# Kernel tuning notes

Hardware: AMD Instinct MI355X
Metric: run time of the kernel (lower is better)

The kernel has to match this reference:

```python
import jax, jax.numpy as jnp
import numpy as np

B, S, D, H, DK, F = 8, 1024, 1024, 16, 64, 4096
EPS = 1e-5


def _layer_norm(x, g, b):
    mu = jnp.mean(x, axis=-1, keepdims=True)
    var = jnp.var(x, axis=-1, keepdims=True)
    return (x - mu) * jax.lax.rsqrt(var + EPS) * g + b


def setup_inputs() -> dict:
    key = jax.random.key(0)
    ks = jax.random.split(key, 16)
    s = lambda fan: 1.0 / np.sqrt(fan)
    return {
        "src": jax.random.normal(ks[0], (B, S, D), dtype=jnp.float32),
        "Wq": jax.random.uniform(ks[1], (H, D, DK), jnp.float32, -s(D), s(D)),
        "bq": jnp.zeros((H, DK), jnp.float32),
        "Wk": jax.random.uniform(ks[2], (H, D, DK), jnp.float32, -s(D), s(D)),
        "bk": jnp.zeros((H, DK), jnp.float32),
        "Wv": jax.random.uniform(ks[3], (H, D, DK), jnp.float32, -s(D), s(D)),
        "bv": jnp.zeros((H, DK), jnp.float32),
        "Wo": jax.random.uniform(ks[4], (H * DK, D), jnp.float32, -s(H * DK), s(H * DK)),
        "bo": jnp.zeros((D,), jnp.float32),
        "g1": jnp.ones((D,), jnp.float32),
        "be1": jnp.zeros((D,), jnp.float32),
        "W1": jax.random.uniform(ks[5], (D, F), jnp.float32, -s(D), s(D)),
        "b1": jnp.zeros((F,), jnp.float32),
        "W2": jax.random.uniform(ks[6], (F, D), jnp.float32, -s(F), s(F)),
        "b2": jnp.zeros((D,), jnp.float32),
        "g2": jnp.ones((D,), jnp.float32),
        "be2": jnp.zeros((D,), jnp.float32),
    }


def reference(src, Wq, bq, Wk, bk, Wv, bv, Wo, bo, g1, be1, W1, b1, W2, b2, g2, be2):
    # Per-head projections (vectorized over the Python head loop of the original)
    q = jnp.einsum("bsd,hdk->bhsk", src, Wq) + bq[:, None, :]
    k = jnp.einsum("bsd,hdk->bhsk", src, Wk) + bk[:, None, :]
    v = jnp.einsum("bsd,hdk->bhsk", src, Wv) + bv[:, None, :]
    scale = 1.0 / jnp.sqrt(jnp.asarray(DK, src.dtype))
    scores = jnp.einsum("bhsk,bhtk->bhst", q, k) * scale  # [B,H,S,S]
    attn = jax.nn.softmax(scores, axis=-1)
    o = jnp.einsum("bhst,bhtk->bhsk", attn, v)
    # torch.cat over heads on last dim -> [B,S,H*DK] with head-major feature order
    o = o.transpose(0, 2, 1, 3).reshape(B, S, H * DK)
    attn_out = o @ Wo + bo
    x = _layer_norm(src + attn_out, g1, be1)  # dropout inactive at inference
    ff = jax.nn.relu(x @ W1 + b1) @ W2 + b2
    return _layer_norm(x + ff, g2, be2)
```

## Files before the change

kernel.cpp:

```cpp
#include <hip/hip_runtime.h>

#define Bq 8
#define Sq 1024
#define Dq 1024
#define Hq 16
#define DKq 64
#define Fq 4096
#define TOK (Bq*Sq)

typedef unsigned short u16;
typedef unsigned int u32;
typedef __bf16 bf16x8 __attribute__((ext_vector_type(8)));
typedef float  f32x4  __attribute__((ext_vector_type(4)));

__device__ __forceinline__ float bf2f(u16 u) {
  u32 x = ((u32)u) << 16;
  float f; __builtin_memcpy(&f, &x, 4); return f;
}
__device__ __forceinline__ u16 f2bf(float f) {
  u32 u; __builtin_memcpy(&u, &f, 4);
  u += 0x7fffu + ((u >> 16) & 1u);
  return (u16)(u >> 16);
}
__device__ __forceinline__ void async16(const u16* g, u16* l) {
  __builtin_amdgcn_global_load_lds(
      (__attribute__((address_space(1))) void*)(g),
      (__attribute__((address_space(3))) void*)(l), 16, 0, 0);
}
__device__ __forceinline__ u16 load_in(const void* p, long idx, u32 fp32) {
  return fp32 ? f2bf(((const float*)p)[idx]) : ((const u16*)p)[idx];
}
__device__ __forceinline__ int swzb(int row, int colb) {
  return row * 128 + (colb ^ ((row & 7) << 4));
}

struct InTab { const void* p[17]; int n[17]; };

__global__ void detect_all(InTab tab, u32* flags) {
  __shared__ int sh[3][256];
  int bi = blockIdx.x;
  const u16* buf = (const u16*)tab.p[bi];
  long n = tab.n[bi];
  long m = n < 65536 ? n : 65536;
  int t = threadIdx.x;
  int nanpat = 0, evz = 0, oddnz = 0;
  for (long i = t; i < m; i += 256) {
    u16 v = buf[i];
    if ((v & 0x7F80u) == 0x7F80u) nanpat++;
    if ((i & 1) == 0) { if (v == 0) evz++; }
    else { if (v != 0) oddnz++; }
  }
  sh[0][t] = nanpat; sh[1][t] = evz; sh[2][t] = oddnz;
  __syncthreads();
  for (int s = 128; s > 0; s >>= 1) {
    if (t < s) { sh[0][t] += sh[0][t+s]; sh[1][t] += sh[1][t+s]; sh[2][t] += sh[2][t+s]; }
    __syncthreads();
  }
  if (t == 0) {
    long half = m / 2;
    bool fp32 = (sh[0][0] > 8) ||
                (sh[1][0] > (half * 9) / 10 && sh[2][0] > (half * 9) / 10);
    flags[bi] = fp32 ? 1u : 0u;
  }
}

__global__ void diag_ws_too_small(u16* out, float code) { out[0] = f2bf(code); }

__global__ void diag_mixed(const u32* flags, void* out) {
  u32 a = flags[0];
  if (flags[1] != a || flags[7] != a || flags[11] != a || flags[13] != a) {
    if (a) ((float*)out)[0] = 3000.0f;
    else ((u16*)out)[0] = f2bf(3000.0f);
  }
}

__global__ __launch_bounds__(256) void pack_all(const void* __restrict__ Wq,
                                                const void* __restrict__ Wk,
                                                const void* __restrict__ Wv,
                                                const void* __restrict__ Wo,
                                                const void* __restrict__ W1,
                                                const void* __restrict__ W2,
                                                u16* __restrict__ Wqkv_t,
                                                u16* __restrict__ Wo_t,
                                                u16* __restrict__ W1_t,
                                                u16* __restrict__ W2_t,
                                                const u32* __restrict__ flags) {
  int id = blockIdx.x;
  const void* in; u16* out; u32 f; int R, C; long zin; int r0, c0;
  if (id < 768) {
    int w = id >> 8, t = id & 255;
    int z = t >> 4, xt = t & 15;
    in = (w == 0) ? Wq : ((w == 1) ? Wk : Wv);
    f = flags[(w == 0) ? 1 : ((w == 1) ? 3 : 5)];
    R = 1024; C = 64;
    zin = (long)z * 65536;
    out = Wqkv_t + (long)w * 1048576 + (long)z * 65536;
    r0 = xt * 64; c0 = 0;
  } else if (id < 1024) {
    int t = id - 768; int xt = t & 15, yt = t >> 4;
    in = Wo; f = flags[7]; R = 1024; C = 1024; zin = 0; out = Wo_t;
    r0 = xt * 64; c0 = yt * 64;
  } else if (id < 2048) {
    int t = id - 1024; int xt = t & 15, yt = t >> 4;
    in = W1; f = flags[11]; R = 1024; C = 4096; zin = 0; out = W1_t;
    r0 = xt * 64; c0 = yt * 64;
  } else {
    int t = id - 2048; int xt = t & 63, yt = t >> 6;
    in = W2; f = flags[13]; R = 4096; C = 1024; zin = 0; out = W2_t;
    r0 = xt * 64; c0 = yt * 64;
  }
  __shared__ u16 tile[64][65];
  int tx = threadIdx.x & 63, ty = threadIdx.x >> 6;
#pragma unroll
  for (int it = 0; it < 16; it++) {
    int row = it * 4 + ty;
    tile[row][tx] = load_in(in, zin + (long)(r0 + row) * C + (c0 + tx), f);
  }
  __syncthreads();
#pragma unroll
  for (int it = 0; it < 16; it++) {
    int cc = it * 4 + ty;
    out[(long)(c0 + cc) * R + r0 + tx] = tile[tx][cc];
  }
}

struct CvtTab { const void* p[10]; int flagidx[10]; int dstoff[10]; int n[10]; };
__global__ void cvt_small(CvtTab tab, u16* __restrict__ dst, const u32* __restrict__ flags) {
  int e = blockIdx.x;
  u32 f = flags[tab.flagidx[e]];
  const void* p = tab.p[e];
  int n = tab.n[e], o = tab.dstoff[e];
  for (int i = threadIdx.x; i < n; i += 256) dst[o + i] = load_in(p, i, f);
}

__global__ __launch_bounds__(256) void cvt_src(const void* __restrict__ in,
                                               u16* __restrict__ out,
                                               const u32* __restrict__ flag) {
  u32 f = *flag;
  long i8 = ((long)blockIdx.x * 256 + threadIdx.x) * 8;
  if (f) {
    const float4* f4 = (const float4*)((const float*)in + i8);
    float4 a = f4[0], b = f4[1];
    u16 v[8] = {f2bf(a.x), f2bf(a.y), f2bf(a.z), f2bf(a.w),
                f2bf(b.x), f2bf(b.y), f2bf(b.z), f2bf(b.w)};
    *(uint4*)(out + i8) = *(const uint4*)v;
  } else {
    *(uint4*)(out + i8) = *(const uint4*)((const u16*)in + i8);
  }
}

__global__ __launch_bounds__(256) void gemm_bt(const u16* __restrict__ A,
                                               const u16* __restrict__ Bt,
                                               const u16* __restrict__ bias,
                                               u16* __restrict__ C,
                                               int M, int N, int K, int act,
                                               int ldc) {
  __shared__ alignas(16) u16 sA[2][128 * 32];
  __shared__ alignas(16) u16 sB[2][128 * 32];
  const int tid = threadIdx.x;
  const int wv = tid >> 6, lane = tid & 63;
  const int m16 = lane & 15, quad = lane >> 4;
  const long bm = (long)blockIdx.x * 128;
  const long bn = (long)blockIdx.y * 128;
  const int wm = (wv >> 1) * 64, wn = (wv & 1) * 64;

  f32x4 acc[4][4];
#pragma unroll
  for (int i = 0; i < 4; i++)
#pragma unroll
    for (int j = 0; j < 4; j++) acc[i][j] = (f32x4){0.f, 0.f, 0.f, 0.f};

  const int row_s = tid >> 2;
  const int col_s = (tid & 3) * 8;
  const u16* gA0 = A + (bm + row_s) * (long)K + col_s;
  const u16* gA1 = gA0 + 64 * (long)K;
  const u16* gB0 = Bt + (bn + row_s) * (long)K + col_s;
  const u16* gB1 = gB0 + 64 * (long)K;

  auto stage = [&](int p, int k) {
    async16(gA0 + k, &sA[p][wv * 512]);
    async16(gA1 + k, &sA[p][2048 + wv * 512]);
    async16(gB0 + k, &sB[p][wv * 512]);
    async16(gB1 + k, &sB[p][2048 + wv * 512]);
  };
  auto compute = [&](int p) {
    bf16x8 af[4], bf_[4];
#pragma unroll
    for (int mi = 0; mi < 4; mi++)
      af[mi] = *(const bf16x8*)&sA[p][(wm + mi * 16 + m16) * 32 + quad * 8];
#pragma unroll
    for (int ni = 0; ni < 4; ni++)
      bf_[ni] = *(const bf16x8*)&sB[p][(wn + ni * 16 + m16) * 32 + quad * 8];
#pragma unroll
    for (int mi = 0; mi < 4; mi++)
#pragma unroll
      for (int ni = 0; ni < 4; ni++)
        acc[mi][ni] = __builtin_amdgcn_mfma_f32_16x16x32_bf16(af[mi], bf_[ni], acc[mi][ni], 0, 0, 0);
  };

  stage(0, 0);
  for (int k0 = 0; k0 < K; k0 += 64) {
    __syncthreads();
    if (k0 + 32 < K) stage(1, k0 + 32);
    compute(0);
    __syncthreads();
    if (k0 + 64 < K) stage(0, k0 + 64);
    compute(1);
  }

  float bv4[4];
#pragma unroll
  for (int ni = 0; ni < 4; ni++) bv4[ni] = bf2f(bias[bn + wn + ni * 16 + m16]);

#pragma unroll
  for (int mi = 0; mi < 4; mi++) {
#pragma unroll
    for (int ni = 0; ni < 4; ni++) {
      long col = bn + wn + ni * 16 + m16;
      long rowb = bm + wm + mi * 16 + quad * 4;
#pragma unroll
      for (int r = 0; r < 4; r++) {
        float v = acc[mi][ni][r] + bv4[ni];
        if (act) v = fmaxf(v, 0.f);
        C[(rowb + r) * (long)ldc + col] = f2bf(v);
      }
    }
  }
}

#define MF16 __builtin_amdgcn_mfma_f32_16x16x32_bf16

#define TILE256(BUF, NBUF, DOA, DOB, KA, KB, VMS)                              \
  {                                                                            \
                   \
    _Pragma("unroll") for (int mi = 0; mi < 4; mi++)                           \
      _Pragma("unroll") for (int kk = 0; kk < 2; kk++)                         \
        afr[mi][kk] = *(const bf16x8*)&sA[BUF][offA + mi * 1024 + kof[kk]];    \
    _Pragma("unroll") for (int ni = 0; ni < 2; ni++)                           \
      _Pragma("unroll") for (int kk = 0; kk < 2; kk++)                         \
        bfr[ni][kk] = *(const bf16x8*)&sB[BUF][offB + ni * 1024 + kof[kk]];    \
    if (DOA) stA(NBUF, 0, KA);                                                 \
    __builtin_amdgcn_s_barrier();                                              \
    asm volatile("s_waitcnt lgkmcnt(0)");                                      \
    __builtin_amdgcn_s_setprio(1);                                             \
    _Pragma("unroll") for (int kk = 0; kk < 2; kk++)                           \
      _Pragma("unroll") for (int mi = 0; mi < 4; mi++)                         \
        _Pragma("unroll") for (int ni = 0; ni < 2; ni++)                       \
          acc[mi][ni] = MF16(afr[mi][kk], bfr[ni][kk], acc[mi][ni], 0, 0, 0);  \
    __builtin_amdgcn_s_setprio(0);                                             \
    __builtin_amdgcn_s_barrier();                                              \
                                 \
    _Pragma("unroll") for (int ni = 0; ni < 2; ni++)                           \
      _Pragma("unroll") for (int kk = 0; kk < 2; kk++)                         \
        bfr[2 + ni][kk] = *(const bf16x8*)&sB[BUF][offB + (2 + ni) * 1024 + kof[kk]]; \
    if (DOA) stA(NBUF, 1, KA);                                                 \
    __builtin_amdgcn_s_barrier();                                              \
    asm volatile("s_waitcnt lgkmcnt(0)");                                      \
    __builtin_amdgcn_s_setprio(1);                                             \
    _Pragma("unroll") for (int kk = 0; kk < 2; kk++)                           \
      _Pragma("unroll") for (int mi = 0; mi < 4; mi++)                         \
        _Pragma("unroll") for (int ni = 0; ni < 2; ni++)                       \
          acc[mi][2 + ni] = MF16(afr[mi][kk], bfr[2 + ni][kk], acc[mi][2 + ni], 0, 0, 0); \
    __builtin_amdgcn_s_setprio(0);                                             \
    __builtin_amdgcn_s_barrier();                                              \
     \
    _Pragma("unroll") for (int mi = 0; mi < 4; mi++)                           \
      _Pragma("unroll") for (int kk = 0; kk < 2; kk++)                         \
        afr[mi][kk] = *(const bf16x8*)&sA[BUF][offA + (4 + mi) * 1024 + kof[kk]]; \
    if (DOB) stB(BUF, 0, KB);                                                  \
    __builtin_amdgcn_s_barrier();                                              \
    asm volatile("s_waitcnt lgkmcnt(0)");                                      \
    __builtin_amdgcn_s_setprio(1);                                             \
    _Pragma("unroll") for (int kk = 0; kk < 2; kk++)                           \
      _Pragma("unroll") for (int mi = 0; mi < 4; mi++)                         \
        _Pragma("unroll") for (int ni = 0; ni < 2; ni++)                       \
          acc[4 + mi][2 + ni] = MF16(afr[mi][kk], bfr[2 + ni][kk], acc[4 + mi][2 + ni], 0, 0, 0); \
    __builtin_amdgcn_s_setprio(0);                                             \
    __builtin_amdgcn_s_barrier();                                              \
           \
    if (DOB) stB(BUF, 1, KB);                                                  \
    asm volatile("s_waitcnt vmcnt(" VMS ")" ::: "memory");                     \
    __builtin_amdgcn_s_barrier();                                              \
    asm volatile("s_waitcnt lgkmcnt(0)");                                      \
    __builtin_amdgcn_s_setprio(1);                                             \
    _Pragma("unroll") for (int kk = 0; kk < 2; kk++)                           \
      _Pragma("unroll") for (int mi = 0; mi < 4; mi++)                         \
        _Pragma("unroll") for (int ni = 0; ni < 2; ni++)                       \
          acc[4 + mi][ni] = MF16(afr[mi][kk], bfr[ni][kk], acc[4 + mi][ni], 0, 0, 0); \
    __builtin_amdgcn_s_setprio(0);                                             \
    __builtin_amdgcn_s_barrier();                                              \
  }

__global__ __launch_bounds__(512, 2) void gemm256(const u16* __restrict__ A,
                                                  const u16* __restrict__ Bt,
                                                  const u16* __restrict__ bias,
                                                  u16* __restrict__ C,
                                                  int M, int N, int K, int act,
                                                  int ldc, u16* __restrict__ Vt,
                                                  int mode) {
  __shared__ alignas(16) u16 sA[2][16384];
  __shared__ alignas(16) u16 sB[2][16384];
  const int tid = threadIdx.x;
  const int wv = tid >> 6, lane = tid & 63;
  const int m16 = lane & 15, quad = lane >> 4;
  const int wr = wv >> 2, wc = wv & 3;

  const int NT = N >> 8;
  int bid = blockIdx.x;
  {
    const int nwg = gridDim.x;
    const int q = nwg >> 3, r = nwg & 7;
    const int xcd = bid & 7, lp = bid >> 3;
    bid = (xcd < r ? xcd * (q + 1) : r * (q + 1) + (xcd - r) * q) + lp;
  }
  const long bm = (long)(bid / NT) * 256;
  const long bn = (long)(bid % NT) * 256;

  const int r0 = wv * 16 + (lane >> 3);
  const int cstg = ((lane & 7) ^ (lane >> 3)) * 8;
  const u16* gA0 = A  + (bm + r0) * (long)K + cstg;
  const u16* gA1 = A  + (bm + 128 + r0) * (long)K + cstg;
  const u16* gB0 = Bt + (bn + r0) * (long)K + cstg;
  const u16* gB1 = Bt + (bn + 128 + r0) * (long)K + cstg;
  const long k8 = 8 * (long)K;

  auto stA = [&](int nb, int h, int k0) {
    const u16* s = (h ? gA1 : gA0) + k0;
    u16* d = &sA[nb][h * 8192 + wv * 1024];
    async16(s, d);
    async16(s + k8, d + 512);
  };
  auto stB = [&](int nb, int h, int k0) {
    const u16* s = (h ? gB1 : gB0) + k0;
    u16* d = &sB[nb][h * 8192 + wv * 1024];
    async16(s, d);
    async16(s + k8, d + 512);
  };

  const int qs = quad ^ (m16 & 3);
  const int hb = (m16 >> 2) & 1;
  const int kof[2] = {hb * 32, 32 - hb * 32};
  const int offA = wr * 8192 + m16 * 64 + qs * 8;
  const int offB = (wc >> 1) * 8192 + (wc & 1) * 4096 + m16 * 64 + qs * 8;

  f32x4 acc[8][4];
#pragma unroll
  for (int i = 0; i < 8; i++)
#pragma unroll
    for (int j = 0; j < 4; j++) acc[i][j] = (f32x4){0.f, 0.f, 0.f, 0.f};
  bf16x8 afr[4][2], bfr[4][2];

  const int KT = K >> 6;

  stA(0, 0, 0); stA(0, 1, 0); stB(0, 0, 0); stB(0, 1, 0);
  stB(1, 0, 64); stB(1, 1, 64);
  asm volatile("s_waitcnt vmcnt(4)" ::: "memory");
  __builtin_amdgcn_s_barrier();

  int T = 0;
  for (; T + 2 < KT; T += 2) {
    const int kA1 = (T + 1) << 6, kB2 = (T + 2) << 6, kB3 = (T + 3) << 6;
    TILE256(0, 1, true, true, kA1, kB2, "4");
    TILE256(1, 0, true, true, kB2, kB3, "4");
  }
  {
    const int kA1 = (T + 1) << 6;
    TILE256(0, 1, true, false, kA1, 0, "0");
    TILE256(1, 0, false, false, 0, 0, "0");
  }

  float bv4[4];
#pragma unroll
  for (int ni = 0; ni < 4; ni++) bv4[ni] = bf2f(bias[bn + wc * 64 + ni * 16 + m16]);

#pragma unroll
  for (int mi = 0; mi < 8; mi++) {
#pragma unroll
    for (int ni = 0; ni < 4; ni++) {
      long col = bn + wc * 64 + ni * 16 + m16;
      long rowb = bm + wr * 128 + mi * 16 + quad * 4;
      if (mode == 1 && col >= 2048) {
        int hh = ((int)col >> 6) & 15, dk = (int)col & 63;
        int bb = (int)(rowb >> 10), ss = (int)(rowb & 1023);
        u16 t4[4];
#pragma unroll
        for (int r = 0; r < 4; r++) t4[r] = f2bf(acc[mi][ni][r] + bv4[ni]);
        *(uint2*)&Vt[(((long)bb * 16 + hh) * 64 + dk) * 1024 + ss] = *(const uint2*)t4;
      } else {
#pragma unroll
        for (int r = 0; r < 4; r++) {
          float v = acc[mi][ni][r] + bv4[ni];
          if (act) v = fmaxf(v, 0.f);
          C[(rowb + r) * (long)ldc + col] = f2bf(v);
        }
      }
    }
  }
}

#define TILE128(BUF, NBUF, DOA, DOB, KA, KB, VMS)                              \
  {                                                                            \
                           \
    _Pragma("unroll") for (int mi = 0; mi < 4; mi++)                           \
      _Pragma("unroll") for (int kk = 0; kk < 2; kk++)                         \
        afr[mi][kk] = *(const bf16x8*)&sA[BUF][offA + mi * 1024 + kof[kk]];    \
    _Pragma("unroll") for (int ni = 0; ni < 2; ni++)                           \
      _Pragma("unroll") for (int kk = 0; kk < 2; kk++)                         \
        bfr[ni][kk] = *(const bf16x8*)&sB[BUF][offB + ni * 1024 + kof[kk]];    \
    if (DOA) stA(NBUF, 0, KA);                                                 \
    __builtin_amdgcn_s_barrier();                                              \
    asm volatile("s_waitcnt lgkmcnt(0)");                                      \
    __builtin_amdgcn_s_setprio(1);                                             \
    _Pragma("unroll") for (int kk = 0; kk < 2; kk++)                           \
      _Pragma("unroll") for (int mi = 0; mi < 4; mi++)                         \
        _Pragma("unroll") for (int ni = 0; ni < 2; ni++)                       \
          acc[mi][ni] = MF16(afr[mi][kk], bfr[ni][kk], acc[mi][ni], 0, 0, 0);  \
    __builtin_amdgcn_s_setprio(0);                                             \
    __builtin_amdgcn_s_barrier();                                              \
                            \
    _Pragma("unroll") for (int ni = 0; ni < 2; ni++)                           \
      _Pragma("unroll") for (int kk = 0; kk < 2; kk++)                         \
        bfr[2 + ni][kk] = *(const bf16x8*)&sB[BUF][offB + (2 + ni) * 1024 + kof[kk]]; \
    if (DOA) stA(NBUF, 1, KA);                                                 \
    __builtin_amdgcn_s_barrier();                                              \
    asm volatile("s_waitcnt lgkmcnt(0)");                                      \
    __builtin_amdgcn_s_setprio(1);                                             \
    _Pragma("unroll") for (int kk = 0; kk < 2; kk++)                           \
      _Pragma("unroll") for (int mi = 0; mi < 4; mi++)                         \
        _Pragma("unroll") for (int ni = 0; ni < 2; ni++)                       \
          acc[mi][2 + ni] = MF16(afr[mi][kk], bfr[2 + ni][kk], acc[mi][2 + ni], 0, 0, 0); \
    __builtin_amdgcn_s_setprio(0);                                             \
    __builtin_amdgcn_s_barrier();                                              \
                   \
    if (DOB) stB(BUF, KB);                                                     \
    asm volatile("s_waitcnt vmcnt(" VMS ")" ::: "memory");                     \
    __builtin_amdgcn_s_barrier();                                              \
  }

__global__ __launch_bounds__(512, 2) void gemm256x128(const u16* __restrict__ A,
                                                      const u16* __restrict__ Bt,
                                                      const u16* __restrict__ bias,
                                                      u16* __restrict__ C,
                                                      int M, int N, int K, int act) {
  __shared__ alignas(16) u16 sA[2][16384];
  __shared__ alignas(16) u16 sB[2][8192];
  const int tid = threadIdx.x;
  const int wv = tid >> 6, lane = tid & 63;
  const int m16 = lane & 15, quad = lane >> 4;
  const int wr = wv >> 1, wc = wv & 1;

  const int NT = N >> 7;
  int bid = blockIdx.x;
  {
    const int nwg = gridDim.x;
    const int q = nwg >> 3, r = nwg & 7;
    const int xcd = bid & 7, lp = bid >> 3;
    bid = (xcd < r ? xcd * (q + 1) : r * (q + 1) + (xcd - r) * q) + lp;
  }
  const long bm = (long)(bid / NT) * 256;
  const long bn = (long)(bid % NT) * 128;

  const int r0 = wv * 16 + (lane >> 3);
  const int cstg = ((lane & 7) ^ (lane >> 3)) * 8;
  const u16* gA0 = A + (bm + r0) * (long)K + cstg;
  const u16* gA1 = A + (bm + 128 + r0) * (long)K + cstg;
  const u16* gB0 = Bt + (bn + r0) * (long)K + cstg;
  const long k8 = 8 * (long)K;

  auto stA = [&](int nb, int h, int k0) {
    const u16* s = (h ? gA1 : gA0) + k0;
    u16* d = &sA[nb][h * 8192 + wv * 1024];
    async16(s, d);
    async16(s + k8, d + 512);
  };
  auto stB = [&](int nb, int k0) {
    const u16* s = gB0 + k0;
    u16* d = &sB[nb][wv * 1024];
    async16(s, d);
    async16(s + k8, d + 512);
  };

  const int qs = quad ^ (m16 & 3);
  const int hb = (m16 >> 2) & 1;
  const int kof[2] = {hb * 32, 32 - hb * 32};
  const int offA = (wr >> 1) * 8192 + (wr & 1) * 4096 + m16 * 64 + qs * 8;
  const int offB = wc * 4096 + m16 * 64 + qs * 8;

  f32x4 acc[4][4];
#pragma unroll
  for (int i = 0; i < 4; i++)
#pragma unroll
    for (int j = 0; j < 4; j++) acc[i][j] = (f32x4){0.f, 0.f, 0.f, 0.f};
  bf16x8 afr[4][2], bfr[4][2];

  const int KT = K >> 6;

  stA(0, 0, 0); stA(0, 1, 0); stB(0, 0);
  stB(1, 64);
  asm volatile("s_waitcnt vmcnt(2)" ::: "memory");
  __builtin_amdgcn_s_barrier();

  int T = 0;
  for (; T + 2 < KT; T += 2) {
    TILE128(0, 1, true, true, (T + 1) << 6, (T + 2) << 6, "2");
    TILE128(1, 0, true, true, (T + 2) << 6, (T + 3) << 6, "2");
  }
  TILE128(0, 1, true, false, (T + 1) << 6, 0, "0");
  TILE128(1, 0, false, false, 0, 0, "0");

  float bv4[4];
#pragma unroll
  for (int ni = 0; ni < 4; ni++) bv4[ni] = bf2f(bias[bn + wc * 64 + ni * 16 + m16]);

#pragma unroll
  for (int mi = 0; mi < 4; mi++) {
#pragma unroll
    for (int ni = 0; ni < 4; ni++) {
      long col = bn + wc * 64 + ni * 16 + m16;
      long rowb = bm + wr * 64 + mi * 16 + quad * 4;
#pragma unroll
      for (int r = 0; r < 4; r++) {
        float v = acc[mi][ni][r] + bv4[ni];
        if (act) v = fmaxf(v, 0.f);
        C[(rowb + r) * (long)N + col] = f2bf(v);
      }
    }
  }
}

__global__ __launch_bounds__(256, 4) void attn_fwd(const u16* __restrict__ qk,
                                                   const u16* __restrict__ Vt,
                                                   u16* __restrict__ attnO) {
  __shared__ alignas(16) u16 sQP[8192];
  __shared__ alignas(16) u16 sK[4096];
  __shared__ alignas(16) u16 sVt[4096];
  const int tid = threadIdx.x;
  const int bh = blockIdx.x;
  const int qt = blockIdx.y;
  const int b = bh >> 4, h = bh & 15;
  const int wv = tid >> 6, lane = tid & 63;
  const int m16 = lane & 15, quad = lane >> 4;
  const int kk = tid >> 3;
  const int t7 = tid & 7;

  char* cQP = (char*)sQP;
  char* cK = (char*)sK;
  char* cV = (char*)sVt;

  {
    int row = tid >> 1, half = tid & 1;
    const u16* g = qk + (long)(b * Sq + qt * 128 + row) * 2048 + h * 64 + half * 32;
#pragma unroll
    for (int j = 0; j < 4; j++) {
      uint4 raw = *(const uint4*)(g + j * 8);
      const u16* pv = (const u16*)&raw;
      u16 t[8];
#pragma unroll
      for (int e = 0; e < 8; e++) t[e] = f2bf(bf2f(pv[e]) * 0.125f);
      *(uint4*)(cQP + swzb(row, half * 64 + j * 16)) = *(const uint4*)t;
    }
  }
  __syncthreads();
  bf16x8 qf[2][2];
#pragma unroll
  for (int qt2 = 0; qt2 < 2; qt2++)
#pragma unroll
    for (int s = 0; s < 2; s++)
      qf[qt2][s] = *(const bf16x8*)(cQP + swzb(wv * 32 + qt2 * 16 + m16, s * 64 + quad * 16));

  f32x4 o[4][2];
#pragma unroll
  for (int dt = 0; dt < 4; dt++)
#pragma unroll
    for (int qt2 = 0; qt2 < 2; qt2++) o[dt][qt2] = (f32x4){0.f, 0.f, 0.f, 0.f};
  float mrun[2] = {-1e30f, -1e30f}, lrun[2] = {0.f, 0.f};

  const u16* gK = qk + (long)(b * Sq + kk) * 2048 + 1024 + h * 64 + t7 * 8;
  const u16* gV = Vt + ((long)bh * 64 + kk) * 1024 + t7 * 8;
  const long stepK = (long)64 * 2048;
  const int off0 = swzb(kk, t7 * 16);
  const int off1 = off0 + 4096;

  uint4 rk0 = *(const uint4*)gK;
  uint4 rk1 = *(const uint4*)(gK + 32 * 2048);
  uint4 rv0 = *(const uint4*)gV;
  uint4 rv1 = *(const uint4*)(gV + 32 * 1024);

  for (int kt = 0; kt < 16; kt++) {
    __syncthreads();
    *(uint4*)(cK + off0) = rk0;
    *(uint4*)(cK + off1) = rk1;
    *(uint4*)(cV + off0) = rv0;
    *(uint4*)(cV + off1) = rv1;
    __syncthreads();

    f32x4 st[4][2];
#pragma unroll
    for (int kt2 = 0; kt2 < 4; kt2++)
#pragma unroll
      for (int qt2 = 0; qt2 < 2; qt2++) st[kt2][qt2] = (f32x4){0.f, 0.f, 0.f, 0.f};
    __builtin_amdgcn_s_setprio(1);
#pragma unroll
    for (int s = 0; s < 2; s++) {
      bf16x8 kf[4];
#pragma unroll
      for (int kt2 = 0; kt2 < 4; kt2++)
        kf[kt2] = *(const bf16x8*)(cK + swzb(kt2 * 16 + m16, s * 64 + quad * 16));
#pragma unroll
      for (int kt2 = 0; kt2 < 4; kt2++)
#pragma unroll
        for (int qt2 = 0; qt2 < 2; qt2++)
          st[kt2][qt2] = MF16(kf[kt2], qf[qt2][s], st[kt2][qt2], 0, 0, 0);
    }
    __builtin_amdgcn_s_setprio(0);

    if (kt < 15) {
      rk0 = *(const uint4*)(gK + (long)(kt + 1) * stepK);
      rk1 = *(const uint4*)(gK + (long)(kt + 1) * stepK + 32 * 2048);
      rv0 = *(const uint4*)(gV + (kt + 1) * 64);
      rv1 = *(const uint4*)(gV + (kt + 1) * 64 + 32 * 1024);
    }

    char* cP = cQP + wv * 4096;
#pragma unroll
    for (int qt2 = 0; qt2 < 2; qt2++) {
      float pm = st[0][qt2][0];
#pragma unroll
      for (int kt2 = 0; kt2 < 4; kt2++)
#pragma unroll
        for (int r = 0; r < 4; r++) pm = fmaxf(pm, st[kt2][qt2][r]);
      pm = fmaxf(pm, __shfl_xor(pm, 16));
      pm = fmaxf(pm, __shfl_xor(pm, 32));
      float mnew = fmaxf(mrun[qt2], pm);
      float al = __expf(mrun[qt2] - mnew);
      mrun[qt2] = mnew;
      float rs = 0.f;
#pragma unroll
      for (int kt2 = 0; kt2 < 4; kt2++) {
        u16 t4[4];
#pragma unroll
        for (int r = 0; r < 4; r++) {
          float p = __expf(st[kt2][qt2][r] - mnew);
          rs += p;
          t4[r] = f2bf(p);
        }
        *(uint2*)(cP + swzb(qt2 * 16 + m16, kt2 * 32 + quad * 8)) = *(const uint2*)t4;
      }
      rs += __shfl_xor(rs, 16);
      rs += __shfl_xor(rs, 32);
      lrun[qt2] = lrun[qt2] * al + rs;
#pragma unroll
      for (int dt = 0; dt < 4; dt++)
#pragma unroll
        for (int r = 0; r < 4; r++) o[dt][qt2][r] *= al;
    }

    bf16x8 pb[2][2];
#pragma unroll
    for (int qt2 = 0; qt2 < 2; qt2++)
#pragma unroll
      for (int ks = 0; ks < 2; ks++)
        pb[qt2][ks] = *(const bf16x8*)(cP + swzb(qt2 * 16 + m16, ks * 64 + quad * 16));
    __builtin_amdgcn_s_setprio(1);
#pragma unroll
    for (int dt = 0; dt < 4; dt++) {
      bf16x8 v0 = *(const bf16x8*)(cV + swzb(dt * 16 + m16, quad * 16));
      bf16x8 v1 = *(const bf16x8*)(cV + swzb(dt * 16 + m16, 64 + quad * 16));
#pragma unroll
      for (int qt2 = 0; qt2 < 2; qt2++) {
        o[dt][qt2] = MF16(v0, pb[qt2][0], o[dt][qt2], 0, 0, 0);
        o[dt][qt2] = MF16(v1, pb[qt2][1], o[dt][qt2], 0, 0, 0);
      }
    }
    __builtin_amdgcn_s_setprio(0);
  }

#pragma unroll
  for (int qt2 = 0; qt2 < 2; qt2++) {
    float rl = 1.f / lrun[qt2];
    long tok = (long)(b * Sq + qt * 128 + wv * 32 + qt2 * 16 + m16);
#pragma unroll
    for (int dt = 0; dt < 4; dt++) {
      u16 t4[4];
#pragma unroll
      for (int r = 0; r < 4; r++) t4[r] = f2bf(o[dt][qt2][r] * rl);
      *(uint2*)&attnO[tok * 1024 + h * 64 + dt * 16 + quad * 4] = *(const uint2*)t4;
    }
  }
}

__global__ __launch_bounds__(256) void add_ln(const u16* __restrict__ X,
                                              const u16* __restrict__ Y,
                                              const u16* __restrict__ g,
                                              const u16* __restrict__ be,
                                              u16* __restrict__ out) {
  const int row = blockIdx.x;
  const int t = threadIdx.x;
  const long base = (long)row * Dq;
  const int i4 = t * 4;
  uint2 xr = *(const uint2*)&X[base + i4];
  uint2 yr = *(const uint2*)&Y[base + i4];
  const u16* xp = (const u16*)&xr;
  const u16* yp = (const u16*)&yr;
  float v[4]; float s = 0.f, ss = 0.f;
#pragma unroll
  for (int i = 0; i < 4; i++) {
    float x = bf2f(xp[i]) + bf2f(yp[i]);
    v[i] = x; s += x; ss += x * x;
  }
#pragma unroll
  for (int off = 32; off > 0; off >>= 1) { s += __shfl_down(s, off); ss += __shfl_down(ss, off); }
  __shared__ float red[8];
  int wv = t >> 6, ln = t & 63;
  if (ln == 0) { red[wv] = s; red[4 + wv] = ss; }
  __syncthreads();
  s = red[0] + red[1] + red[2] + red[3];
  ss = red[4] + red[5] + red[6] + red[7];
  float mean = s * (1.f / Dq);
  float var = ss * (1.f / Dq) - mean * mean;
  float rstd = rsqrtf(var + 1e-5f);
  uint2 gr = *(const uint2*)&g[i4];
  uint2 br = *(const uint2*)&be[i4];
  const u16* gp = (const u16*)&gr;
  const u16* bp = (const u16*)&br;
  u16 o4[4];
#pragma unroll
  for (int i = 0; i < 4; i++)
    o4[i] = f2bf((v[i] - mean) * rstd * bf2f(gp[i]) + bf2f(bp[i]));
  *(uint2*)&out[base + i4] = *(const uint2*)o4;
}

__global__ __launch_bounds__(256) void add_ln_out(const u16* __restrict__ X,
                                                  const u16* __restrict__ Y,
                                                  const u16* __restrict__ g,
                                                  const u16* __restrict__ be,
                                                  void* __restrict__ out,
                                                  const u32* __restrict__ outflag) {
  const u32 fp32 = *outflag;
  const int row = blockIdx.x;
  const int t = threadIdx.x;
  const long base = (long)row * Dq;
  const int i4 = t * 4;
  uint2 xr = *(const uint2*)&X[base + i4];
  uint2 yr = *(const uint2*)&Y[base + i4];
  const u16* xp = (const u16*)&xr;
  const u16* yp = (const u16*)&yr;
  float v[4]; float s = 0.f, ss = 0.f;
#pragma unroll
  for (int i = 0; i < 4; i++) {
    float x = bf2f(xp[i]) + bf2f(yp[i]);
    v[i] = x; s += x; ss += x * x;
  }
#pragma unroll
  for (int off = 32; off > 0; off >>= 1) { s += __shfl_down(s, off); ss += __shfl_down(ss, off); }
  __shared__ float red[8];
  int wv = t >> 6, ln = t & 63;
  if (ln == 0) { red[wv] = s; red[4 + wv] = ss; }
  __syncthreads();
  s = red[0] + red[1] + red[2] + red[3];
  ss = red[4] + red[5] + red[6] + red[7];
  float mean = s * (1.f / Dq);
  float var = ss * (1.f / Dq) - mean * mean;
  float rstd = rsqrtf(var + 1e-5f);
  uint2 gr = *(const uint2*)&g[i4];
  uint2 br = *(const uint2*)&be[i4];
  const u16* gp = (const u16*)&gr;
  const u16* bp = (const u16*)&br;
  if (fp32) {
    float4 o4;
    o4.x = (v[0] - mean) * rstd * bf2f(gp[0]) + bf2f(bp[0]);
    o4.y = (v[1] - mean) * rstd * bf2f(gp[1]) + bf2f(bp[1]);
    o4.z = (v[2] - mean) * rstd * bf2f(gp[2]) + bf2f(bp[2]);
    o4.w = (v[3] - mean) * rstd * bf2f(gp[3]) + bf2f(bp[3]);
    *(float4*)((float*)out + base + i4) = o4;
  } else {
    u16 o4[4];
#pragma unroll
    for (int i = 0; i < 4; i++)
      o4[i] = f2bf((v[i] - mean) * rstd * bf2f(gp[i]) + bf2f(bp[i]));
    *(uint2*)((u16*)out + base + i4) = *(const uint2*)o4;
  }
}

extern "C" void kernel_launch(void* const* d_in, const int* in_sizes, int n_in,
                              void* d_out, int out_size, void* d_ws, size_t ws_size,
                              hipStream_t stream) {
  char* ws = (char*)d_ws;
  size_t off = 0;
  auto alloc = [&](size_t bytes) {
    void* p = ws + off;
    off += (bytes + 255) & ~(size_t)255;
    return p;
  };
  u32* flags  = (u32*)alloc(32 * 4);
  u16* Wqkv_t = (u16*)alloc((size_t)3072 * 1024 * 2);
  u16* Wo_t   = (u16*)alloc((size_t)1024 * 1024 * 2);
  u16* W1_t   = (u16*)alloc((size_t)4096 * 1024 * 2);
  u16* W2_t   = (u16*)alloc((size_t)1024 * 4096 * 2);
  u16* svec   = (u16*)alloc((size_t)13312 * 2);
  u16* src_bf = (u16*)alloc((size_t)TOK * 1024 * 2);
  u16* regA   = (u16*)alloc((size_t)TOK * 4096 * 2);
  size_t need_chunk2 = off;
  size_t need_full   = off + (size_t)TOK * 4096 * 2 / 2;

  u16* outw = (u16*)d_out;
  int CH;
  if (ws_size >= need_full) { CH = 8192; (void)alloc((size_t)32 << 20); }
  else if (ws_size >= need_chunk2) CH = 4096;
  else if (ws_size >= need_chunk2 - ((size_t)16 << 20)) CH = 2048;
  else {
    diag_ws_too_small<<<1, 1, 0, stream>>>(outw, 8000.0f + (float)(ws_size >> 20));
    return;
  }

  u16* qk    = regA;
  u16* Vt    = regA + (size_t)TOK * 2048;
  u16* attnb = regA + (size_t)TOK * 3072;
  u16* proj  = regA;
  u16* x     = regA + (size_t)TOK * 1024;
  u16* h1    = regA + (size_t)TOK * 2048;
  u16* f2    = src_bf;

  u16* bqkv = svec + 0;
  u16* bo_c = svec + 3072;
  u16* g1_c = svec + 4096;
  u16* be1_c = svec + 5120;
  u16* b1_c = svec + 6144;
  u16* b2_c = svec + 10240;
  u16* g2_c = svec + 11264;
  u16* be2_c = svec + 12288;

  InTab itab;
  for (int i = 0; i < 17; i++) { itab.p[i] = d_in[i]; itab.n[i] = in_sizes[i]; }
  detect_all<<<dim3(17), 256, 0, stream>>>(itab, flags);

  pack_all<<<dim3(3072), 256, 0, stream>>>(d_in[1], d_in[3], d_in[5], d_in[7], d_in[11], d_in[13],
                                           Wqkv_t, Wo_t, W1_t, W2_t, flags);

  CvtTab ct;
  const int srcs[10] = {2, 4, 6, 8, 9, 10, 12, 14, 15, 16};
  const int offs[10] = {0, 1024, 2048, 3072, 4096, 5120, 6144, 10240, 11264, 12288};
  const int lens[10] = {1024, 1024, 1024, 1024, 1024, 1024, 4096, 1024, 1024, 1024};
  for (int e = 0; e < 10; e++) { ct.p[e] = d_in[srcs[e]]; ct.flagidx[e] = srcs[e]; ct.dstoff[e] = offs[e]; ct.n[e] = lens[e]; }
  cvt_small<<<dim3(10), 256, 0, stream>>>(ct, svec, flags);

  cvt_src<<<dim3(TOK * 1024 / (256 * 8)), 256, 0, stream>>>(d_in[0], src_bf, &flags[0]);

  gemm256<<<dim3(32 * 12), 512, 0, stream>>>(src_bf, Wqkv_t, bqkv, qk, TOK, 3072, 1024, 0,
                                             2048, Vt, 1);
  attn_fwd<<<dim3(128, 8), 256, 0, stream>>>(qk, Vt, attnb);
  gemm256x128<<<dim3(256), 512, 0, stream>>>(attnb, Wo_t, bo_c, proj, TOK, 1024, 1024, 0);
  add_ln<<<dim3(TOK), 256, 0, stream>>>(src_bf, proj, g1_c, be1_c, x);
  for (int c = 0; c < TOK / CH; c++) {
    const u16* xc = x + (size_t)c * CH * 1024;
    u16* f2c = f2 + (size_t)c * CH * 1024;
    if (CH >= 4096) {
      gemm256<<<dim3((CH / 256) * 16), 512, 0, stream>>>(xc, W1_t, b1_c, h1, CH, 4096, 1024, 1,
                                                         4096, nullptr, 0);
    } else {
      gemm_bt<<<dim3(CH / 128, 32), 256, 0, stream>>>(xc, W1_t, b1_c, h1, CH, 4096, 1024, 1, 4096);
    }
    if (CH == 8192) {
      gemm256x128<<<dim3((CH / 256) * 8), 512, 0, stream>>>(h1, W2_t, b2_c, f2c, CH, 1024, 4096, 0);
    } else {
      gemm_bt<<<dim3(CH / 128, 8), 256, 0, stream>>>(h1, W2_t, b2_c, f2c, CH, 1024, 4096, 0, 1024);
    }
  }
  add_ln_out<<<dim3(TOK), 256, 0, stream>>>(x, f2, g2_c, be2_c, d_out, &flags[0]);
  diag_mixed<<<1, 1, 0, stream>>>(flags, d_out);
}
```

Measured before the change: 573.5 us.

## Use exp2 softmax with lazy rescaling and vectorize weight transpose loads

Folds log2(e) into the Q pre-scale so the online softmax uses exp2f instead of __expf. Skips the running-max update and the rescaling of the output accumulator unless some lane's new block max exceeds the running max by more than a threshold, which removes most per-tile multiplies. Separately, the weight transpose kernel now loads 16 contiguous elements per thread with vector loads instead of scalar strided loads. The lazy rescale lets probabilities exceed 1 (up to about 2^11.5) before bf16 conversion, which may cost some accuracy.

```diff
diff --git a/kernel.cpp b/kernel.cpp
--- a/kernel.cpp
+++ b/kernel.cpp
@@ -110,13 +110,29 @@
     r0 = xt * 64; c0 = yt * 64;
   }
   __shared__ u16 tile[64][65];
+  {
+    int row = threadIdx.x >> 2;
+    int cg  = (threadIdx.x & 3) << 4;
+    long srcidx = zin + (long)(r0 + row) * C + (c0 + cg);
+    u16 tv[16];
+    if (f) {
+      const float4* p4 = (const float4*)((const float*)in + srcidx);
+#pragma unroll
+      for (int j = 0; j < 4; j++) {
+        float4 v = p4[j];
+        tv[j * 4 + 0] = f2bf(v.x); tv[j * 4 + 1] = f2bf(v.y);
+        tv[j * 4 + 2] = f2bf(v.z); tv[j * 4 + 3] = f2bf(v.w);
+      }
+    } else {
+      const uint4* p8 = (const uint4*)((const u16*)in + srcidx);
+      *(uint4*)&tv[0] = p8[0];
+      *(uint4*)&tv[8] = p8[1];
+    }
+#pragma unroll
+    for (int j = 0; j < 16; j++) tile[row][cg + j] = tv[j];
+  }
+  __syncthreads();
   int tx = threadIdx.x & 63, ty = threadIdx.x >> 6;
-#pragma unroll
-  for (int it = 0; it < 16; it++) {
-    int row = it * 4 + ty;
-    tile[row][tx] = load_in(in, zin + (long)(r0 + row) * C + (c0 + tx), f);
-  }
-  __syncthreads();
 #pragma unroll
   for (int it = 0; it < 16; it++) {
     int cc = it * 4 + ty;
@@ -556,7 +572,7 @@
       const u16* pv = (const u16*)&raw;
       u16 t[8];
 #pragma unroll
-      for (int e = 0; e < 8; e++) t[e] = f2bf(bf2f(pv[e]) * 0.125f);
+      for (int e = 0; e < 8; e++) t[e] = f2bf(bf2f(pv[e]) * 0.1803368801f);
       *(uint4*)(cQP + swzb(row, half * 64 + j * 16)) = *(const uint4*)t;
     }
   }
@@ -631,16 +647,23 @@
         for (int r = 0; r < 4; r++) pm = fmaxf(pm, st[kt2][qt2][r]);
       pm = fmaxf(pm, __shfl_xor(pm, 16));
       pm = fmaxf(pm, __shfl_xor(pm, 32));
-      float mnew = fmaxf(mrun[qt2], pm);
-      float al = __expf(mrun[qt2] - mnew);
-      mrun[qt2] = mnew;
+      if (!__all(pm - mrun[qt2] <= 11.5f)) {
+        float mnew = fmaxf(mrun[qt2], pm);
+        float al = exp2f(mrun[qt2] - mnew);
+        mrun[qt2] = mnew;
+        lrun[qt2] *= al;
+#pragma unroll
+        for (int dt = 0; dt < 4; dt++)
+#pragma unroll
+          for (int r = 0; r < 4; r++) o[dt][qt2][r] *= al;
+      }
       float rs = 0.f;
 #pragma unroll
       for (int kt2 = 0; kt2 < 4; kt2++) {
         u16 t4[4];
 #pragma unroll
         for (int r = 0; r < 4; r++) {
-          float p = __expf(st[kt2][qt2][r] - mnew);
+          float p = exp2f(st[kt2][qt2][r] - mrun[qt2]);
           rs += p;
           t4[r] = f2bf(p);
         }
@@ -648,11 +671,7 @@
       }
       rs += __shfl_xor(rs, 16);
       rs += __shfl_xor(rs, 32);
-      lrun[qt2] = lrun[qt2] * al + rs;
-#pragma unroll
-      for (int dt = 0; dt < 4; dt++)
-#pragma unroll
-        for (int r = 0; r < 4; r++) o[dt][qt2][r] *= al;
+      lrun[qt2] += rs;
     }
 
     bf16x8 pb[2][2];
```

Result: no change. 568.1 us (-0.9%).
